# Optimization experiments

Hardware: AMD Instinct MI355X
Metric: run time of the kernel (lower is better)

The kernel has to match this reference:

```python
import jax, jax.numpy as jnp
import numpy as np

N = 100000   # every_node
IN = 128     # in_channels
OUT = 128    # out_channels
R = 8        # every_relation
B = 4        # num_bases
E = 1_600_000  # total edges (avg degree 16)
E_PER = E // R
LEAKY_SLOPE = 0.2


def _xavier_uniform(key, shape, gain):
    fan_in, fan_out = shape[-2], shape[-1]
    bound = gain * np.sqrt(6.0 / (fan_in + fan_out))
    return jax.random.uniform(key, shape, jnp.float32, -bound, bound)


def setup_inputs() -> dict:
    key = jax.random.key(0)
    k = jax.random.split(key, 6)
    gain = float(np.sqrt(2.0))  # calculate_gain('relu')
    node_embeddings = jax.random.normal(k[0], (N, IN), jnp.float32)
    src = jax.random.randint(k[1], (E,), 0, N, jnp.int32)
    dst = jax.random.randint(k[2], (E,), 0, N, jnp.int32)
    rel = jnp.repeat(jnp.arange(R, dtype=jnp.int32), E_PER)  # sorted by relation
    triples = jnp.stack([src, rel, dst], axis=1)  # [E,3] = (src, rel, dst)
    change_points = jnp.arange(0, E + 1, E_PER, dtype=jnp.int32)  # [R+1]
    basis = _xavier_uniform(k[3], (B, IN, OUT), gain)
    att = _xavier_uniform(k[4], (R, B), gain)
    attention = _xavier_uniform(k[5], (R, 2 * OUT), gain)
    bias = jnp.zeros((OUT,), jnp.float32)
    return {
        'node_embeddings': node_embeddings,
        'triples': triples,
        'change_points': change_points,
        'basis': basis,
        'att': att,
        'attention': attention,
        'bias': bias,
    }


def reference(node_embeddings, triples, change_points, basis, att, attention, bias):
    # Basis decomposition: per-relation weight, then per-relation transformed features.
    weights = jnp.einsum('rb,bio->rio', att, basis)              # [R, in, out]
    Wh = jnp.einsum('rio,ni->rno', weights, node_embeddings)     # [R, N, out]

    src, rel, dst = triples[:, 0], triples[:, 2], None  # placeholder; see below
    src = triples[:, 0]
    rel = triples[:, 1]   # triples are sorted by relation; rel column == block id from change_points
    dst = triples[:, 2]

    # Attention score a . [Wh_src || Wh_dst] decomposed into per-node partial scores.
    a_src = attention[:, :OUT]                                   # [R, out]
    a_dst = attention[:, OUT:]                                   # [R, out]
    s_src = jnp.einsum('rno,ro->rn', Wh, a_src)                  # [R, N]
    s_dst = jnp.einsum('rno,ro->rn', Wh, a_dst)                  # [R, N]
    e_raw = jax.nn.leaky_relu(s_src[rel, src] + s_dst[rel, dst], LEAKY_SLOPE)  # [E]

    # Segment softmax per (relation, dst) — matches per-relation scatter amax/add.
    seg = rel.astype(jnp.int32) * N + dst.astype(jnp.int32)
    e_max = jax.ops.segment_max(e_raw, seg, num_segments=R * N)
    e_exp = jnp.exp(e_raw - e_max[seg])
    denom = jax.ops.segment_sum(e_exp, seg, num_segments=R * N)
    alpha = e_exp / jnp.maximum(denom[seg], 1e-8)                # [E]
    # (attn dropout omitted: eval mode)

    # SpMM aggregation: sum over relations of A_rel @ Wh_rel.
    msgs = alpha[:, None] * Wh[rel, src]                         # [E, out]
    h_prime = jax.ops.segment_sum(msgs, dst, num_segments=N)     # [N, out]

    output = h_prime + bias
    if node_embeddings.shape[-1] == OUT:
        output = output + node_embeddings  # residual
    return output
```

## Files before the change

kernel.cpp:

```cpp
#include <hip/hip_runtime.h>
#include <stdint.h>

#define NN 100000
#define DIM 128
#define RR 8
#define BB 4
#define EE 1600000
#define EPR 200000
#define SLOPE 0.2f
#define CAP 64

typedef __attribute__((ext_vector_type(8))) short short8;
typedef __attribute__((ext_vector_type(4))) float f32x4;

__device__ __forceinline__ unsigned short f2bf(float f) {
    unsigned u = __float_as_uint(f);
    unsigned r = (u + 0x7FFFu + ((u >> 16) & 1u)) >> 16;
    return (unsigned short)r;
}

__global__ void k_prep(const float* __restrict__ att, const float* __restrict__ basis,
                       const float* __restrict__ attention,
                       unsigned short* __restrict__ wt, unsigned short* __restrict__ w16b) {
    int r = blockIdx.x;
    int i = threadIdx.x;
    float a[BB];
#pragma unroll
    for (int b = 0; b < BB; ++b) a[b] = att[r * BB + b];
    const float* asrc = attention + r * 2 * DIM;
    const float* adst = asrc + DIM;
    float ws = 0.f, wd = 0.f;
    for (int o = 0; o < DIM; ++o) {
        float w = 0.f;
#pragma unroll
        for (int b = 0; b < BB; ++b) w += a[b] * basis[(b * DIM + i) * DIM + o];
        wt[(r * DIM + o) * DIM + i] = f2bf(w);
        ws += w * asrc[o];
        wd += w * adst[o];
    }
    w16b[r * DIM + i] = f2bf(ws);
    w16b[(RR + r) * DIM + i] = f2bf(wd);
}

__global__ __launch_bounds__(256) void k_conv(const float* __restrict__ x,
        unsigned* __restrict__ xb, int* __restrict__ cnt) {
    size_t t = (size_t)blockIdx.x * 256 + threadIdx.x;
    float4 v = *(const float4*)(x + t * 4);
    uint2 o;
    o.x = (unsigned)f2bf(v.x) | ((unsigned)f2bf(v.y) << 16);
    o.y = (unsigned)f2bf(v.z) | ((unsigned)f2bf(v.w) << 16);
    *(uint2*)(xb + t * 2) = o;
    if (t < NN) cnt[t] = 0;
}

__global__ __launch_bounds__(256) void k_score16(const unsigned short* __restrict__ w16b,
        const unsigned short* __restrict__ xb, float* __restrict__ ssrc,
        float* __restrict__ sdst) {
    __shared__ unsigned short lw[16 * 136];
    for (int u = threadIdx.x; u < 16 * 16; u += 256) {
        int row = u >> 4, ch = u & 15;
        *(uint4*)&lw[row * 136 + ch * 8] = *(const uint4*)&w16b[row * 128 + ch * 8];
    }
    __syncthreads();
    int wave = threadIdx.x >> 6, lane = threadIdx.x & 63;
    int ncol = blockIdx.x * 64 + wave * 16 + (lane & 15);
    int nc = ncol < NN ? ncol : NN - 1;
    int kg = (lane >> 4) * 8;
    const short8* xrow = (const short8*)(xb + (size_t)nc * DIM);
    f32x4 acc = (f32x4){0.f, 0.f, 0.f, 0.f};
#pragma unroll
    for (int k = 0; k < 4; ++k) {
        short8 a = *(const short8*)&lw[(lane & 15) * 136 + k * 32 + kg];
        short8 b = xrow[k * 4 + (lane >> 4)];
        acc = __builtin_amdgcn_mfma_f32_16x16x32_bf16(a, b, acc, 0, 0, 0);
    }
    if (ncol < NN) {
#pragma unroll
        for (int j = 0; j < 4; ++j) {
            int row = (lane >> 4) * 4 + j;
            if (row < RR) ssrc[row * NN + ncol] = acc[j];
            else sdst[(row - RR) * NN + ncol] = acc[j];
        }
    }
}

__global__ __launch_bounds__(256) void k_gemm(const unsigned short* __restrict__ wt,
        const unsigned short* __restrict__ xb, unsigned short* __restrict__ wh) {
    __shared__ unsigned short lwt[DIM * 136];
    int r = blockIdx.y;
    {
        const uint4* src = (const uint4*)(wt + r * DIM * DIM);
        for (int u = threadIdx.x; u < DIM * DIM / 8; u += 256) {
            int row = u >> 4, ch = u & 15;
            *(uint4*)&lwt[row * 136 + ch * 8] = src[u];
        }
    }
    __syncthreads();
    int wave = threadIdx.x >> 6, lane = threadIdx.x & 63;
    int ncol = blockIdx.x * 64 + wave * 16 + (lane & 15);
    int kg = (lane >> 4) * 8;
    int nc = ncol < NN ? ncol : NN - 1;
    const short8* xrow = (const short8*)(xb + (size_t)nc * DIM);
    short8 bfrag[4];
#pragma unroll
    for (int k = 0; k < 4; ++k) bfrag[k] = xrow[k * 4 + (lane >> 4)];
    f32x4 acc[8];
#pragma unroll
    for (int f = 0; f < 8; ++f) acc[f] = (f32x4){0.f, 0.f, 0.f, 0.f};
#pragma unroll
    for (int k = 0; k < 4; ++k) {
#pragma unroll
        for (int f = 0; f < 8; ++f) {
            short8 a = *(const short8*)&lwt[(f * 16 + (lane & 15)) * 136 + k * 32 + kg];
            acc[f] = __builtin_amdgcn_mfma_f32_16x16x32_bf16(a, bfrag[k], acc[f], 0, 0, 0);
        }
    }
    if (ncol < NN) {
        size_t base = ((size_t)r * NN + ncol) * DIM;
#pragma unroll
        for (int f = 0; f < 8; ++f) {
            uint2 v;
            v.x = (unsigned)f2bf(acc[f][0]) | ((unsigned)f2bf(acc[f][1]) << 16);
            v.y = (unsigned)f2bf(acc[f][2]) | ((unsigned)f2bf(acc[f][3]) << 16);
            *(uint2*)&wh[base + f * 16 + (lane >> 4) * 4] = v;
        }
    }
}

__global__ __launch_bounds__(256) void k_edge(const int* __restrict__ tri,
        const float* __restrict__ ssrc, const float* __restrict__ sdst,
        int* __restrict__ cnt, unsigned* __restrict__ bucket) {
    int e = blockIdx.x * 256 + threadIdx.x;
    int src = tri[3 * e], dst = tri[3 * e + 2];
    int rel = e / EPR;
    float er = ssrc[rel * NN + src] + sdst[rel * NN + dst];
    er = er > 0.f ? er : SLOPE * er;
    int q = (int)fmaf(er, 64.f, 2048.5f);
    q = q < 0 ? 0 : (q > 4095 ? 4095 : q);
    int pos = atomicAdd(&cnt[dst], 1);
    if (pos < CAP)
        bucket[(size_t)dst * CAP + pos] =
            (unsigned)src | ((unsigned)rel << 17) | ((unsigned)q << 20);
}

__global__ __launch_bounds__(256, 8) void k_agg(const int* __restrict__ cnt,
        const unsigned* __restrict__ bucket, const unsigned* __restrict__ whu,
        const float* __restrict__ x, const float* __restrict__ bias,
        float* __restrict__ out) {
    int tid = threadIdx.x;
    int wave = tid >> 6, lane = tid & 63;
    int d = blockIdx.x * 4 + wave;
    int c = min(cnt[d], CAP);
    unsigned mv = 0;
    if (lane < c) mv = bucket[(size_t)d * CAP + lane];
    int rel = (int)((mv >> 17) & 7);
    float pl = (lane < c) ? __expf(fmaf((float)(mv >> 20), 0.015625f, -32.0f)) : 0.f;
    float sd[RR];
#pragma unroll
    for (int r = 0; r < RR; ++r) {
        float t = (rel == r) ? pl : 0.f;
#pragma unroll
        for (int o = 32; o > 0; o >>= 1) t += __shfl_xor(t, o);
        sd[r] = t;
    }
    float s = sd[0];
#pragma unroll
    for (int r = 1; r < RR; ++r) s = (rel == r) ? sd[r] : s;
    float al = pl * __builtin_amdgcn_rcpf(fmaxf(s, 1e-8f));

    float a0 = 0.f, a1 = 0.f;
    for (int j0 = 0; j0 < c; j0 += 8) {
        unsigned w[8];
        float av[8];
#pragma unroll
        for (int u = 0; u < 8; ++u) {
            unsigned mx = (unsigned)__shfl((int)mv, j0 + u);
            av[u] = __shfl(al, j0 + u);
            int row = (int)((mx >> 17) & 7) * NN + (int)(mx & 0x1FFFF);
            w[u] = whu[(size_t)row * 64 + lane];
        }
#pragma unroll
        for (int u = 0; u < 8; ++u) {
            a0 = fmaf(av[u], __uint_as_float(w[u] << 16), a0);
            a1 = fmaf(av[u], __uint_as_float(w[u] & 0xFFFF0000u), a1);
        }
    }
    float2 xv = *(const float2*)(x + (size_t)d * DIM + lane * 2);
    float2 bv = *(const float2*)(bias + lane * 2);
    float2 ov;
    ov.x = a0 + xv.x + bv.x;
    ov.y = a1 + xv.y + bv.y;
    *(float2*)(out + (size_t)d * DIM + lane * 2) = ov;
}

extern "C" void kernel_launch(void* const* d_in, const int* in_sizes, int n_in,
                              void* d_out, int out_size, void* d_ws, size_t ws_size,
                              hipStream_t stream) {
    const float* x = (const float*)d_in[0];
    const int* tri = (const int*)d_in[1];
    const float* basis = (const float*)d_in[3];
    const float* att = (const float*)d_in[4];
    const float* attention = (const float*)d_in[5];
    const float* bias = (const float*)d_in[6];
    float* out = (float*)d_out;

    char* ws = (char*)d_ws;
    size_t off = 0;
    auto alloc = [&](size_t b) {
        char* p = ws + off;
        off = (off + b + 255) & ~(size_t)255;
        return p;
    };
    unsigned short* wh = (unsigned short*)alloc((size_t)RR * NN * DIM * 2);
    unsigned* xb = (unsigned*)alloc((size_t)NN * DIM * 2);
    unsigned short* wt = (unsigned short*)alloc((size_t)RR * DIM * DIM * 2);
    unsigned short* w16b = (unsigned short*)alloc((size_t)16 * DIM * 2);
    float* ssrc = (float*)alloc((size_t)RR * NN * 4);
    float* sdst = (float*)alloc((size_t)RR * NN * 4);
    int* cnt = (int*)alloc((size_t)NN * 4);
    unsigned* bucket = (unsigned*)alloc((size_t)NN * CAP * 4);

    k_prep<<<RR, DIM, 0, stream>>>(att, basis, attention, wt, w16b);
    k_conv<<<NN * DIM / 4 / 256, 256, 0, stream>>>(x, xb, cnt);
    k_score16<<<(NN + 63) / 64, 256, 0, stream>>>(w16b, (const unsigned short*)xb,
                                                  ssrc, sdst);
    k_gemm<<<dim3((NN + 63) / 64, RR), 256, 0, stream>>>(wt, (const unsigned short*)xb, wh);
    k_edge<<<EE / 256, 256, 0, stream>>>(tri, ssrc, sdst, cnt, bucket);
    k_agg<<<NN / 4, 256, 0, stream>>>(cnt, bucket, (const unsigned*)wh, x, bias, out);
}
```

Before: 320.3 us.

## Merge independent kernels into combined launches and stage GEMM output through LDS

Folds k_prep into k_conv as extra blocks of a single k_pre launch. Merges the per-relation GEMM and the edge scoring/bucketing kernel into one k_main launch, so the two independent workloads can overlap on the GPU. Interleaves the relation index into the block id so blocks sharing x rows run close together, and writes GEMM results through LDS for coalesced 16-byte stores. This trades launch gaps and tail idle time for extra LDS syncs and a larger heterogeneous grid, and the cheap k_prep work now sits in the same launch as the conversion.

```diff
diff --git a/kernel.cpp b/kernel.cpp
--- a/kernel.cpp
+++ b/kernel.cpp
@@ -9,6 +9,9 @@
 #define EPR 200000
 #define SLOPE 0.2f
 #define CAP 64
+#define NCONV 12500
+#define NBG 12504
+#define NBE 6250
 
 typedef __attribute__((ext_vector_type(8))) short short8;
 typedef __attribute__((ext_vector_type(4))) float f32x4;
@@ -19,38 +22,42 @@
     return (unsigned short)r;
 }
 
-__global__ void k_prep(const float* __restrict__ att, const float* __restrict__ basis,
-                       const float* __restrict__ attention,
-                       unsigned short* __restrict__ wt, unsigned short* __restrict__ w16b) {
-    int r = blockIdx.x;
-    int i = threadIdx.x;
-    float a[BB];
-#pragma unroll
-    for (int b = 0; b < BB; ++b) a[b] = att[r * BB + b];
-    const float* asrc = attention + r * 2 * DIM;
-    const float* adst = asrc + DIM;
-    float ws = 0.f, wd = 0.f;
-    for (int o = 0; o < DIM; ++o) {
-        float w = 0.f;
-#pragma unroll
-        for (int b = 0; b < BB; ++b) w += a[b] * basis[(b * DIM + i) * DIM + o];
-        wt[(r * DIM + o) * DIM + i] = f2bf(w);
-        ws += w * asrc[o];
-        wd += w * adst[o];
-    }
-    w16b[r * DIM + i] = f2bf(ws);
-    w16b[(RR + r) * DIM + i] = f2bf(wd);
-}
-
-__global__ __launch_bounds__(256) void k_conv(const float* __restrict__ x,
-        unsigned* __restrict__ xb, int* __restrict__ cnt) {
-    size_t t = (size_t)blockIdx.x * 256 + threadIdx.x;
-    float4 v = *(const float4*)(x + t * 4);
-    uint2 o;
-    o.x = (unsigned)f2bf(v.x) | ((unsigned)f2bf(v.y) << 16);
-    o.y = (unsigned)f2bf(v.z) | ((unsigned)f2bf(v.w) << 16);
-    *(uint2*)(xb + t * 2) = o;
-    if (t < NN) cnt[t] = 0;
+__global__ __launch_bounds__(256) void k_pre(const float* __restrict__ x,
+        unsigned* __restrict__ xb, int* __restrict__ cnt,
+        const float* __restrict__ att, const float* __restrict__ basis,
+        const float* __restrict__ attention, unsigned short* __restrict__ wt,
+        unsigned short* __restrict__ w16b) {
+    int bid = blockIdx.x;
+    if (bid < NCONV) {
+        size_t t = (size_t)bid * 256 + threadIdx.x;
+        float4 v = *(const float4*)(x + t * 4);
+        uint2 o;
+        o.x = (unsigned)f2bf(v.x) | ((unsigned)f2bf(v.y) << 16);
+        o.y = (unsigned)f2bf(v.z) | ((unsigned)f2bf(v.w) << 16);
+        *(uint2*)(xb + t * 2) = o;
+        if (t < NN) cnt[t] = 0;
+    } else {
+        int r = bid - NCONV;
+        int i = threadIdx.x;
+        if (i < DIM) {
+            float a[BB];
+#pragma unroll
+            for (int b = 0; b < BB; ++b) a[b] = att[r * BB + b];
+            const float* asrc = attention + r * 2 * DIM;
+            const float* adst = asrc + DIM;
+            float ws = 0.f, wd = 0.f;
+            for (int o = 0; o < DIM; ++o) {
+                float w = 0.f;
+#pragma unroll
+                for (int b = 0; b < BB; ++b) w += a[b] * basis[(b * DIM + i) * DIM + o];
+                wt[(r * DIM + o) * DIM + i] = f2bf(w);
+                ws += w * asrc[o];
+                wd += w * adst[o];
+            }
+            w16b[r * DIM + i] = f2bf(ws);
+            w16b[(RR + r) * DIM + i] = f2bf(wd);
+        }
+    }
 }
 
 __global__ __launch_bounds__(256) void k_score16(const unsigned short* __restrict__ w16b,
@@ -84,63 +91,76 @@
     }
 }
 
-__global__ __launch_bounds__(256) void k_gemm(const unsigned short* __restrict__ wt,
-        const unsigned short* __restrict__ xb, unsigned short* __restrict__ wh) {
-    __shared__ unsigned short lwt[DIM * 136];
-    int r = blockIdx.y;
-    {
-        const uint4* src = (const uint4*)(wt + r * DIM * DIM);
-        for (int u = threadIdx.x; u < DIM * DIM / 8; u += 256) {
-            int row = u >> 4, ch = u & 15;
-            *(uint4*)&lwt[row * 136 + ch * 8] = src[u];
-        }
-    }
-    __syncthreads();
-    int wave = threadIdx.x >> 6, lane = threadIdx.x & 63;
-    int ncol = blockIdx.x * 64 + wave * 16 + (lane & 15);
-    int kg = (lane >> 4) * 8;
-    int nc = ncol < NN ? ncol : NN - 1;
-    const short8* xrow = (const short8*)(xb + (size_t)nc * DIM);
-    short8 bfrag[4];
-#pragma unroll
-    for (int k = 0; k < 4; ++k) bfrag[k] = xrow[k * 4 + (lane >> 4)];
-    f32x4 acc[8];
-#pragma unroll
-    for (int f = 0; f < 8; ++f) acc[f] = (f32x4){0.f, 0.f, 0.f, 0.f};
-#pragma unroll
-    for (int k = 0; k < 4; ++k) {
-#pragma unroll
-        for (int f = 0; f < 8; ++f) {
-            short8 a = *(const short8*)&lwt[(f * 16 + (lane & 15)) * 136 + k * 32 + kg];
-            acc[f] = __builtin_amdgcn_mfma_f32_16x16x32_bf16(a, bfrag[k], acc[f], 0, 0, 0);
-        }
-    }
-    if (ncol < NN) {
-        size_t base = ((size_t)r * NN + ncol) * DIM;
+__global__ __launch_bounds__(256) void k_main(const unsigned short* __restrict__ wt,
+        const unsigned short* __restrict__ xb, unsigned short* __restrict__ wh,
+        const int* __restrict__ tri, const float* __restrict__ ssrc,
+        const float* __restrict__ sdst, int* __restrict__ cnt,
+        unsigned* __restrict__ bucket) {
+    __shared__ unsigned short lds[DIM * 136];
+    int bid = blockIdx.x;
+    if (bid < NBG) {
+        int r = bid & 7;
+        int ncol0 = (bid >> 3) * 64;
+        {
+            const uint4* src = (const uint4*)(wt + r * DIM * DIM);
+            for (int u = threadIdx.x; u < DIM * DIM / 8; u += 256) {
+                int row = u >> 4, ch = u & 15;
+                *(uint4*)&lds[row * 136 + ch * 8] = src[u];
+            }
+        }
+        __syncthreads();
+        int wave = threadIdx.x >> 6, lane = threadIdx.x & 63;
+        int ncol = ncol0 + wave * 16 + (lane & 15);
+        int kg = (lane >> 4) * 8;
+        int nc = ncol < NN ? ncol : NN - 1;
+        const short8* xrow = (const short8*)(xb + (size_t)nc * DIM);
+        short8 bfrag[4];
+#pragma unroll
+        for (int k = 0; k < 4; ++k) bfrag[k] = xrow[k * 4 + (lane >> 4)];
+        f32x4 acc[8];
+#pragma unroll
+        for (int f = 0; f < 8; ++f) acc[f] = (f32x4){0.f, 0.f, 0.f, 0.f};
+#pragma unroll
+        for (int k = 0; k < 4; ++k) {
+#pragma unroll
+            for (int f = 0; f < 8; ++f) {
+                short8 a = *(const short8*)&lds[(f * 16 + (lane & 15)) * 136 + k * 32 + kg];
+                acc[f] = __builtin_amdgcn_mfma_f32_16x16x32_bf16(a, bfrag[k], acc[f], 0, 0, 0);
+            }
+        }
+        __syncthreads();
+        int lr = wave * 16 + (lane & 15);
+        int cg = (lane >> 4) * 4;
 #pragma unroll
         for (int f = 0; f < 8; ++f) {
             uint2 v;
             v.x = (unsigned)f2bf(acc[f][0]) | ((unsigned)f2bf(acc[f][1]) << 16);
             v.y = (unsigned)f2bf(acc[f][2]) | ((unsigned)f2bf(acc[f][3]) << 16);
-            *(uint2*)&wh[base + f * 16 + (lane >> 4) * 4] = v;
-        }
-    }
-}
-
-__global__ __launch_bounds__(256) void k_edge(const int* __restrict__ tri,
-        const float* __restrict__ ssrc, const float* __restrict__ sdst,
-        int* __restrict__ cnt, unsigned* __restrict__ bucket) {
-    int e = blockIdx.x * 256 + threadIdx.x;
-    int src = tri[3 * e], dst = tri[3 * e + 2];
-    int rel = e / EPR;
-    float er = ssrc[rel * NN + src] + sdst[rel * NN + dst];
-    er = er > 0.f ? er : SLOPE * er;
-    int q = (int)fmaf(er, 64.f, 2048.5f);
-    q = q < 0 ? 0 : (q > 4095 ? 4095 : q);
-    int pos = atomicAdd(&cnt[dst], 1);
-    if (pos < CAP)
-        bucket[(size_t)dst * CAP + pos] =
-            (unsigned)src | ((unsigned)rel << 17) | ((unsigned)q << 20);
+            *(uint2*)&lds[lr * 132 + f * 16 + cg] = v;
+        }
+        __syncthreads();
+        for (int it = 0; it < 4; ++it) {
+            int idx = it * 256 + threadIdx.x;
+            int row = idx >> 4, ch = idx & 15;
+            int n = ncol0 + row;
+            if (n < NN) {
+                *(uint4*)&wh[((size_t)r * NN + n) * DIM + ch * 8] =
+                    *(const uint4*)&lds[row * 132 + ch * 8];
+            }
+        }
+    } else {
+        int e = (bid - NBG) * 256 + threadIdx.x;
+        int src = tri[3 * e], dst = tri[3 * e + 2];
+        int rel = e / EPR;
+        float er = ssrc[rel * NN + src] + sdst[rel * NN + dst];
+        er = er > 0.f ? er : SLOPE * er;
+        int q = (int)fmaf(er, 64.f, 2048.5f);
+        q = q < 0 ? 0 : (q > 4095 ? 4095 : q);
+        int pos = atomicAdd(&cnt[dst], 1);
+        if (pos < CAP)
+            bucket[(size_t)dst * CAP + pos] =
+                (unsigned)src | ((unsigned)rel << 17) | ((unsigned)q << 20);
+    }
 }
 
 __global__ __launch_bounds__(256, 8) void k_agg(const int* __restrict__ cnt,
@@ -220,11 +240,10 @@
     int* cnt = (int*)alloc((size_t)NN * 4);
     unsigned* bucket = (unsigned*)alloc((size_t)NN * CAP * 4);
 
-    k_prep<<<RR, DIM, 0, stream>>>(att, basis, attention, wt, w16b);
-    k_conv<<<NN * DIM / 4 / 256, 256, 0, stream>>>(x, xb, cnt);
+    k_pre<<<NCONV + RR, 256, 0, stream>>>(x, xb, cnt, att, basis, attention, wt, w16b);
     k_score16<<<(NN + 63) / 64, 256, 0, stream>>>(w16b, (const unsigned short*)xb,
                                                   ssrc, sdst);
-    k_gemm<<<dim3((NN + 63) / 64, RR), 256, 0, stream>>>(wt, (const unsigned short*)xb, wh);
-    k_edge<<<EE / 256, 256, 0, stream>>>(tri, ssrc, sdst, cnt, bucket);
+    k_main<<<NBG + NBE, 256, 0, stream>>>(wt, (const unsigned short*)xb, wh,
+                                          tri, ssrc, sdst, cnt, bucket);
     k_agg<<<NN / 4, 256, 0, stream>>>(cnt, bucket, (const unsigned*)wh, x, bias, out);
 }
```

Measured after the change: 278.2 us. 1.15x faster.
